# Optimization experiments

Measured on AMD Instinct MI355X. Metric: run time of the kernel, lower is better.

## Reference

```python
import jax, jax.numpy as jnp
import numpy as np

L, B, S, D, H, FF = 6, 6, 7, 512, 8, 2048  # layers, support-set size+1, nodes(1 verb + 6 nouns), dim, heads, ffn
HD = D // H


def setup_inputs() -> dict:
    key = jax.random.key(0)
    ks = jax.random.split(key, 16)
    n = lambda k, shape: jax.random.normal(k, shape, dtype=jnp.float32) * 0.02
    z = lambda shape: jnp.zeros(shape, jnp.float32)
    o = lambda shape: jnp.ones(shape, jnp.float32)
    return {
        'features': jax.random.normal(ks[0], (B, S, D), dtype=jnp.float32),
        'role_tokens': jax.random.normal(ks[1], (B, S - 1, D), dtype=jnp.float32),
        'in_w': n(ks[2], (L, 3 * D, D)), 'in_b': z((L, 3 * D)),
        'out_w': n(ks[3], (L, D, D)), 'out_b': z((L, D)),
        'ln1_w': o((L, D)), 'ln1_b': z((L, D)),
        'ln2_w': o((L, D)), 'ln2_b': z((L, D)),
        'ln3_w': o((L, D)), 'ln3_b': z((L, D)),
        'ln4_w': o((L, D)), 'ln4_b': z((L, D)),
        'f1_w1': n(ks[4], (L, FF, D)), 'f1_b1': z((L, FF)),
        'f1_w2': n(ks[5], (L, D, FF)), 'f1_b2': z((L, D)),
        'f2_w1': n(ks[6], (L, FF, D)), 'f2_b1': z((L, FF)),
        'f2_w2': n(ks[7], (L, D, FF)), 'f2_b2': z((L, D)),
        'a1_w': n(ks[8], (L, D, D * 5)), 'a1_b': z((L, D)),
        'a2_w': n(ks[9], (L, D, D * 6)), 'a2_b': z((L, D)),
    }


def _ln(x, w, b):
    mu = jnp.mean(x, -1, keepdims=True)
    var = jnp.mean(jnp.square(x - mu), -1, keepdims=True)
    return (x - mu) * jax.lax.rsqrt(var + 1e-5) * w + b


def _forward(features, role_tokens, in_w, in_b, out_w, out_b, ln1_w, ln1_b, ln2_w, ln2_b,
             ln3_w, ln3_b, ln4_w, ln4_b, f1_w1, f1_b1, f1_w2, f1_b2, f2_w1, f2_b1,
             f2_w2, f2_b2, a1_w, a1_b, a2_w, a2_b):
    def step(x, p):
        (iw, ib, ow, ob, l1w, l1b, l2w, l2b, l3w, l3b, l4w, l4b,
         w11, b11, w12, b12, w21, b21, w22, b22, aw1, ab1, aw2, ab2) = p
        # batched tiny self-attention over the 7 nodes of each of the 6 support examples
        src = x.at[:, 1:, :].add(role_tokens)                      # role embed on noun slots only
        qkv = jnp.einsum('bsd,ed->bse', src, iw) + ib              # (B,S,3D)
        q, k, v = jnp.split(qkv, 3, axis=-1)
        q = q.reshape(B, S, H, HD); k = k.reshape(B, S, H, HD); v = v.reshape(B, S, H, HD)
        att = jax.nn.softmax(jnp.einsum('bqhd,bkhd->bhqk', q, k) / jnp.sqrt(jnp.float32(HD)), axis=-1)
        ctx = jnp.einsum('bhqk,bkhd->bqhd', att, v).reshape(B, S, D)
        msg = jnp.einsum('bsd,ed->bse', ctx, ow) + ob              # (B,S,D)
        verb_msg = msg[:, 0, :]                                    # (B,D)
        noun_msg = msg[:, 1:, :]                                   # (B,S-1,D)
        # gated concat-aggregation
        agg_verb = jax.nn.sigmoid(verb_msg[1:].reshape(-1) @ aw1.T + ab1)  # (D,) from 5 support verb msgs
        agg_noun = jax.nn.sigmoid(noun_msg[0].reshape(-1) @ aw2.T + ab2)   # (D,) from 6 target noun msgs
        # noun update for target example (index 0)
        s = _ln(x[0, 1:, :] + agg_verb, l1w, l1b)                  # (6,D)
        s = _ln(s + (jax.nn.relu(s @ w11.T + b11) @ w12.T + b12), l2w, l2b)
        # verb update for target example
        t = _ln(x[0, 0, :] + agg_noun, l3w, l3b)                   # (D,)
        t = _ln(t + (jax.nn.relu(t @ w21.T + b21) @ w22.T + b22), l4w, l4b)
        new_self = jnp.concatenate([t[None, :], s], axis=0)        # (S,D)
        return jnp.concatenate([new_self[None], x[1:]], axis=0), None

    params = (in_w, in_b, out_w, out_b, ln1_w, ln1_b, ln2_w, ln2_b, ln3_w, ln3_b,
              ln4_w, ln4_b, f1_w1, f1_b1, f1_w2, f1_b2, f2_w1, f2_b1, f2_w2, f2_b2,
              a1_w, a1_b, a2_w, a2_b)
    out, _ = jax.lax.scan(step, features, params)
    return out[0:1]                                                # (1,7,512)


def reference(features, role_tokens, in_w, in_b, out_w, out_b, ln1_w, ln1_b, ln2_w, ln2_b,
              ln3_w, ln3_b, ln4_w, ln4_b, f1_w1, f1_b1, f1_w2, f1_b2, f2_w1, f2_b1,
              f2_w2, f2_b2, a1_w, a1_b, a2_w, a2_b):
    return _forward(features, role_tokens, in_w, in_b, out_w, out_b, ln1_w, ln1_b,
                    ln2_w, ln2_b, ln3_w, ln3_b, ln4_w, ln4_b, f1_w1, f1_b1, f1_w2, f1_b2,
                    f2_w1, f2_b1, f2_w2, f2_b2, a1_w, a1_b, a2_w, a2_b)
```

## Files before the change

kernel.cpp:

```cpp
#include <hip/hip_runtime.h>
#include <math.h>

#define NL 6
#define NB 6
#define NS 7
#define ND 512
#define NH 8
#define HDIM 64
#define NFF 2048
#define NROWS (NB*NS)

__device__ __forceinline__ float wave_sum(float v) {
    v += __shfl_down(v, 32, 64);
    v += __shfl_down(v, 16, 64);
    v += __shfl_down(v, 8, 64);
    v += __shfl_down(v, 4, 64);
    v += __shfl_down(v, 2, 64);
    v += __shfl_down(v, 1, 64);
    return v;
}

__device__ __forceinline__ float dot512(const float* __restrict__ a,
                                        const float* __restrict__ b, int lane) {
    int d0 = lane * 8;
    float4 a1 = *(const float4*)(a + d0);
    float4 a2 = *(const float4*)(a + d0 + 4);
    float4 b1 = *(const float4*)(b + d0);
    float4 b2 = *(const float4*)(b + d0 + 4);
    return a1.x*b1.x + a1.y*b1.y + a1.z*b1.z + a1.w*b1.w
         + a2.x*b2.x + a2.y*b2.y + a2.z*b2.z + a2.w*b2.w;
}

__global__ void qkv_kernel(const float* __restrict__ features,
                           const float* __restrict__ role,
                           const float* __restrict__ cur,
                           const float* __restrict__ iw,
                           const float* __restrict__ ib,
                           float* __restrict__ qkv) {
    int gw = (blockIdx.x * blockDim.x + threadIdx.x) >> 6;
    int lane = threadIdx.x & 63;
    if (gw >= NROWS * 1536) return;
    int row = gw / 1536;
    int e = gw - row * 1536;
    int b = row / NS, s = row - b * NS;
    const float* src = (b == 0) ? (cur + s * ND) : (features + row * ND);
    int d0 = lane * 8;
    float4 s1 = *(const float4*)(src + d0);
    float4 s2 = *(const float4*)(src + d0 + 4);
    if (s > 0) {
        const float* rp = role + (b * (NS-1) + (s-1)) * ND + d0;
        float4 r1 = *(const float4*)(rp);
        float4 r2 = *(const float4*)(rp + 4);
        s1.x += r1.x; s1.y += r1.y; s1.z += r1.z; s1.w += r1.w;
        s2.x += r2.x; s2.y += r2.y; s2.z += r2.z; s2.w += r2.w;
    }
    const float* wr = iw + e * ND + d0;
    float4 w1 = *(const float4*)(wr);
    float4 w2 = *(const float4*)(wr + 4);
    float acc = s1.x*w1.x + s1.y*w1.y + s1.z*w1.z + s1.w*w1.w
              + s2.x*w2.x + s2.y*w2.y + s2.z*w2.z + s2.w*w2.w;
    acc = wave_sum(acc);
    if (lane == 0) qkv[row * 1536 + e] = acc + ib[e];
}

__global__ void attn_kernel(const float* __restrict__ qkv, float* __restrict__ ctx) {
    int b = blockIdx.x >> 3, h = blockIdx.x & 7;
    int lane = threadIdx.x;
    __shared__ float q[NS][HDIM], k[NS][HDIM], v[NS][HDIM], att[NS][NS];
    for (int s = 0; s < NS; s++) {
        const float* base = qkv + (size_t)(b*NS + s) * 1536 + h * HDIM + lane;
        q[s][lane] = base[0];
        k[s][lane] = base[ND];
        v[s][lane] = base[2*ND];
    }
    __syncthreads();
    if (lane < NS*NS) {
        int i = lane / NS, j = lane - (lane / NS) * NS;
        float acc = 0.f;
        for (int d = 0; d < HDIM; d++) acc += q[i][d] * k[j][d];
        att[i][j] = acc * 0.125f;
    }
    __syncthreads();
    if (lane < NS) {
        float m = -1e30f;
        for (int j = 0; j < NS; j++) m = fmaxf(m, att[lane][j]);
        float e[NS]; float sum = 0.f;
        for (int j = 0; j < NS; j++) { e[j] = expf(att[lane][j] - m); sum += e[j]; }
        float inv = 1.f / sum;
        for (int j = 0; j < NS; j++) att[lane][j] = e[j] * inv;
    }
    __syncthreads();
    for (int s = 0; s < NS; s++) {
        float acc = 0.f;
        for (int j = 0; j < NS; j++) acc += att[s][j] * v[j][lane];
        ctx[(size_t)(b*NS + s) * ND + h * HDIM + lane] = acc;
    }
}

__global__ void msg_kernel(const float* __restrict__ ctx,
                           const float* __restrict__ ow,
                           const float* __restrict__ ob,
                           float* __restrict__ msg) {
    int gw = (blockIdx.x * blockDim.x + threadIdx.x) >> 6;
    int lane = threadIdx.x & 63;
    if (gw >= NROWS * ND) return;
    int row = gw / ND, e = gw - row * ND;
    float acc = wave_sum(dot512(ctx + (size_t)row * ND, ow + (size_t)e * ND, lane));
    if (lane == 0) msg[row * ND + e] = acc + ob[e];
}

__global__ void agg_kernel(const float* __restrict__ msg,
                           const float* __restrict__ aw1, const float* __restrict__ ab1,
                           const float* __restrict__ aw2, const float* __restrict__ ab2,
                           float* __restrict__ aggv, float* __restrict__ aggn) {
    int gw = (blockIdx.x * blockDim.x + threadIdx.x) >> 6;
    int lane = threadIdx.x & 63;
    if (gw < ND) {
        int j = gw;
        float acc = 0.f;
        for (int c = 0; c < 5; c++)
            acc += dot512(msg + (size_t)(c+1)*NS*ND, aw1 + (size_t)j*2560 + c*ND, lane);
        acc = wave_sum(acc);
        if (lane == 0) aggv[j] = 1.f / (1.f + expf(-(acc + ab1[j])));
    } else if (gw < 2*ND) {
        int j = gw - ND;
        float acc = 0.f;
        for (int c = 0; c < 6; c++)
            acc += dot512(msg + (size_t)(c+1)*ND, aw2 + (size_t)j*3072 + c*ND, lane);
        acc = wave_sum(acc);
        if (lane == 0) aggn[j] = 1.f / (1.f + expf(-(acc + ab2[j])));
    }
}

__global__ void ln13_kernel(const float* __restrict__ cur,
                            const float* __restrict__ aggv, const float* __restrict__ aggn,
                            const float* __restrict__ l1w, const float* __restrict__ l1b,
                            const float* __restrict__ l3w, const float* __restrict__ l3b,
                            float* __restrict__ xln) {
    int r = blockIdx.x, t = threadIdx.x;
    const float* agg = (r == 0) ? aggn : aggv;
    const float* w   = (r == 0) ? l3w : l1w;
    const float* bb  = (r == 0) ? l3b : l1b;
    float x0 = cur[r*ND + t]       + agg[t];
    float x1 = cur[r*ND + 256 + t] + agg[256 + t];
    __shared__ float sd[4];
    int lane = t & 63, wv = t >> 6;
    float v = wave_sum(x0 + x1);
    if (lane == 0) sd[wv] = v;
    __syncthreads();
    float mu = (sd[0] + sd[1] + sd[2] + sd[3]) * (1.f / ND);
    __syncthreads();
    float d0 = x0 - mu, d1 = x1 - mu;
    v = wave_sum(d0*d0 + d1*d1);
    if (lane == 0) sd[wv] = v;
    __syncthreads();
    float var = (sd[0] + sd[1] + sd[2] + sd[3]) * (1.f / ND);
    float inv = rsqrtf(var + 1e-5f);
    xln[r*ND + t]       = d0 * inv * w[t]     + bb[t];
    xln[r*ND + 256 + t] = d1 * inv * w[256+t] + bb[256+t];
}

__global__ void ffa_kernel(const float* __restrict__ xln,
                           const float* __restrict__ w11, const float* __restrict__ b11,
                           const float* __restrict__ w21, const float* __restrict__ b21,
                           float* __restrict__ h) {
    int gw = (blockIdx.x * blockDim.x + threadIdx.x) >> 6;
    int lane = threadIdx.x & 63;
    if (gw >= NS * NFF) return;
    int r = gw / NFF, f = gw - r * NFF;
    const float* W = (r == 0) ? (w21 + (size_t)f * ND) : (w11 + (size_t)f * ND);
    const float* bias = (r == 0) ? b21 : b11;
    float acc = wave_sum(dot512(xln + r * ND, W, lane));
    if (lane == 0) h[r * NFF + f] = fmaxf(acc + bias[f], 0.f);
}

__global__ void ffb_kernel(const float* __restrict__ xln, const float* __restrict__ hbuf,
                           const float* __restrict__ w12, const float* __restrict__ b12,
                           const float* __restrict__ w22, const float* __restrict__ b22,
                           float* __restrict__ ff) {
    int gw = (blockIdx.x * blockDim.x + threadIdx.x) >> 6;
    int lane = threadIdx.x & 63;
    if (gw >= NS * ND) return;
    int r = gw / ND, d = gw - r * ND;
    const float* W = (r == 0) ? (w22 + (size_t)d * NFF) : (w12 + (size_t)d * NFF);
    const float* bias = (r == 0) ? b22 : b12;
    const float* hin = hbuf + r * NFF;
    float acc = 0.f;
    for (int c = 0; c < 4; c++) acc += dot512(hin + c*ND, W + c*ND, lane);
    acc = wave_sum(acc);
    if (lane == 0) ff[r * ND + d] = xln[r * ND + d] + acc + bias[d];
}

__global__ void ln24_kernel(const float* __restrict__ ff,
                            const float* __restrict__ l2w, const float* __restrict__ l2b,
                            const float* __restrict__ l4w, const float* __restrict__ l4b,
                            float* __restrict__ cur, float* __restrict__ outp) {
    int r = blockIdx.x, t = threadIdx.x;
    const float* w  = (r == 0) ? l4w : l2w;
    const float* bb = (r == 0) ? l4b : l2b;
    float x0 = ff[r*ND + t], x1 = ff[r*ND + 256 + t];
    __shared__ float sd[4];
    int lane = t & 63, wv = t >> 6;
    float v = wave_sum(x0 + x1);
    if (lane == 0) sd[wv] = v;
    __syncthreads();
    float mu = (sd[0] + sd[1] + sd[2] + sd[3]) * (1.f / ND);
    __syncthreads();
    float d0 = x0 - mu, d1 = x1 - mu;
    v = wave_sum(d0*d0 + d1*d1);
    if (lane == 0) sd[wv] = v;
    __syncthreads();
    float var = (sd[0] + sd[1] + sd[2] + sd[3]) * (1.f / ND);
    float inv = rsqrtf(var + 1e-5f);
    float y0 = d0 * inv * w[t]     + bb[t];
    float y1 = d1 * inv * w[256+t] + bb[256+t];
    cur[r*ND + t]       = y0;
    cur[r*ND + 256 + t] = y1;
    if (outp) {
        outp[r*ND + t]       = y0;
        outp[r*ND + 256 + t] = y1;
    }
}

extern "C" void kernel_launch(void* const* d_in, const int* in_sizes, int n_in,
                              void* d_out, int out_size, void* d_ws, size_t ws_size,
                              hipStream_t stream) {
    const float* features = (const float*)d_in[0];
    const float* role     = (const float*)d_in[1];
    const float* in_w  = (const float*)d_in[2];
    const float* in_b  = (const float*)d_in[3];
    const float* out_w = (const float*)d_in[4];
    const float* out_b = (const float*)d_in[5];
    const float* ln1_w = (const float*)d_in[6];
    const float* ln1_b = (const float*)d_in[7];
    const float* ln2_w = (const float*)d_in[8];
    const float* ln2_b = (const float*)d_in[9];
    const float* ln3_w = (const float*)d_in[10];
    const float* ln3_b = (const float*)d_in[11];
    const float* ln4_w = (const float*)d_in[12];
    const float* ln4_b = (const float*)d_in[13];
    const float* f1_w1 = (const float*)d_in[14];
    const float* f1_b1 = (const float*)d_in[15];
    const float* f1_w2 = (const float*)d_in[16];
    const float* f1_b2 = (const float*)d_in[17];
    const float* f2_w1 = (const float*)d_in[18];
    const float* f2_b1 = (const float*)d_in[19];
    const float* f2_w2 = (const float*)d_in[20];
    const float* f2_b2 = (const float*)d_in[21];
    const float* a1_w  = (const float*)d_in[22];
    const float* a1_b  = (const float*)d_in[23];
    const float* a2_w  = (const float*)d_in[24];
    const float* a2_b  = (const float*)d_in[25];

    float* ws   = (float*)d_ws;
    float* cur  = ws;
    float* qkv  = ws + 3584;
    float* ctx  = qkv + 64512;
    float* msg  = ctx + 21504;
    float* aggv = msg + 21504;
    float* aggn = aggv + 512;
    float* xln  = aggn + 512;
    float* hbuf = xln + 3584;
    float* ff   = hbuf + 14336;

    hipMemcpyAsync(cur, features, 3584 * sizeof(float), hipMemcpyDeviceToDevice, stream);

    for (int l = 0; l < NL; l++) {
        qkv_kernel<<<NROWS*1536/4, 256, 0, stream>>>(
            features, role, cur, in_w + (size_t)l*1536*ND, in_b + (size_t)l*1536, qkv);
        attn_kernel<<<NB*NH, 64, 0, stream>>>(qkv, ctx);
        msg_kernel<<<NROWS*ND/4, 256, 0, stream>>>(
            ctx, out_w + (size_t)l*ND*ND, out_b + (size_t)l*ND, msg);
        agg_kernel<<<2*ND/4, 256, 0, stream>>>(
            msg, a1_w + (size_t)l*ND*2560, a1_b + (size_t)l*ND,
                 a2_w + (size_t)l*ND*3072, a2_b + (size_t)l*ND, aggv, aggn);
        ln13_kernel<<<NS, 256, 0, stream>>>(
            cur, aggv, aggn, ln1_w + (size_t)l*ND, ln1_b + (size_t)l*ND,
            ln3_w + (size_t)l*ND, ln3_b + (size_t)l*ND, xln);
        ffa_kernel<<<NS*NFF/4, 256, 0, stream>>>(
            xln, f1_w1 + (size_t)l*NFF*ND, f1_b1 + (size_t)l*NFF,
                 f2_w1 + (size_t)l*NFF*ND, f2_b1 + (size_t)l*NFF, hbuf);
        ffb_kernel<<<NS*ND/4, 256, 0, stream>>>(
            xln, hbuf, f1_w2 + (size_t)l*ND*NFF, f1_b2 + (size_t)l*ND,
                       f2_w2 + (size_t)l*ND*NFF, f2_b2 + (size_t)l*ND, ff);
        ln24_kernel<<<NS, 256, 0, stream>>>(
            ff, ln2_w + (size_t)l*ND, ln2_b + (size_t)l*ND,
                ln4_w + (size_t)l*ND, ln4_b + (size_t)l*ND,
            cur, (l == NL-1) ? (float*)d_out : nullptr);
    }
}
```

Measured before the change: 474.8 us.

## Fuse layernorms into consumers, prune unneeded query rows, fuse attention with out-proj

Removes the separate LN kernels and the device memcpy by recomputing the previous layer's LN2/LN4 inside the qkv, ffa and ffb kernels, with a final LN kernel only at the end. Q projection, attention and out-projection are restricted to the 11 rows whose messages are consumed downstream, and attention is fused with the out-projection via shared memory. FFN kernels now compute several outputs per block from a shared normalized row. This cuts launches and redundant work, at the cost of recomputing LN in many blocks and lower parallelism in the fused attention kernel.

```diff
diff --git a/kernel.cpp b/kernel.cpp
--- a/kernel.cpp
+++ b/kernel.cpp
@@ -10,6 +10,8 @@
 #define NFF 2048
 #define NROWS (NB*NS)
 
+__device__ __constant__ int NRQ[11] = {1,2,3,4,5,6,7,14,21,28,35};
+
 __device__ __forceinline__ float wave_sum(float v) {
     v += __shfl_down(v, 32, 64);
     v += __shfl_down(v, 16, 64);
@@ -17,6 +19,16 @@
     v += __shfl_down(v, 4, 64);
     v += __shfl_down(v, 2, 64);
     v += __shfl_down(v, 1, 64);
+    return v;
+}
+
+__device__ __forceinline__ float wave_sum_all(float v) {
+    v += __shfl_xor(v, 32, 64);
+    v += __shfl_xor(v, 16, 64);
+    v += __shfl_xor(v, 8, 64);
+    v += __shfl_xor(v, 4, 64);
+    v += __shfl_xor(v, 2, 64);
+    v += __shfl_xor(v, 1, 64);
     return v;
 }
 
@@ -31,170 +43,279 @@
          + a2.x*b2.x + a2.y*b2.y + a2.z*b2.z + a2.w*b2.w;
 }
 
-__global__ void qkv_kernel(const float* __restrict__ features,
-                           const float* __restrict__ role,
-                           const float* __restrict__ cur,
-                           const float* __restrict__ iw,
-                           const float* __restrict__ ib,
-                           float* __restrict__ qkv) {
-    int gw = (blockIdx.x * blockDim.x + threadIdx.x) >> 6;
-    int lane = threadIdx.x & 63;
-    if (gw >= NROWS * 1536) return;
-    int row = gw / 1536;
-    int e = gw - row * 1536;
-    int b = row / NS, s = row - b * NS;
-    const float* src = (b == 0) ? (cur + s * ND) : (features + row * ND);
+__device__ __forceinline__ float dot2048(const float* __restrict__ a,
+                                         const float* __restrict__ b, int lane) {
+    float acc = 0.f;
+    for (int c = 0; c < 4; c++) acc += dot512(a + c*ND, b + c*ND, lane);
+    return acc;
+}
+
+__device__ __forceinline__ void load_src(int b, int s, int lane, int l,
+    const float* __restrict__ features, const float* __restrict__ role,
+    const float* __restrict__ ffprev,
+    const float* __restrict__ l2w, const float* __restrict__ l2b,
+    const float* __restrict__ l4w, const float* __restrict__ l4b,
+    float4& s1, float4& s2)
+{
     int d0 = lane * 8;
-    float4 s1 = *(const float4*)(src + d0);
-    float4 s2 = *(const float4*)(src + d0 + 4);
+    if (b > 0 || l == 0) {
+        const float* src = features + (size_t)(b*NS + s) * ND + d0;
+        s1 = *(const float4*)src;
+        s2 = *(const float4*)(src + 4);
+    } else {
+        const float* fp = ffprev + s * ND + d0;
+        float4 f1 = *(const float4*)fp;
+        float4 f2 = *(const float4*)(fp + 4);
+        float sum = f1.x+f1.y+f1.z+f1.w + f2.x+f2.y+f2.z+f2.w;
+        sum = wave_sum_all(sum);
+        float mu = sum * (1.f/ND);
+        f1.x-=mu; f1.y-=mu; f1.z-=mu; f1.w-=mu;
+        f2.x-=mu; f2.y-=mu; f2.z-=mu; f2.w-=mu;
+        float sq = f1.x*f1.x+f1.y*f1.y+f1.z*f1.z+f1.w*f1.w
+                 + f2.x*f2.x+f2.y*f2.y+f2.z*f2.z+f2.w*f2.w;
+        sq = wave_sum_all(sq);
+        float inv = rsqrtf(sq*(1.f/ND) + 1e-5f);
+        const float* w  = (s == 0) ? l4w : l2w;
+        const float* bb = (s == 0) ? l4b : l2b;
+        float4 w1 = *(const float4*)(w + d0),  w2 = *(const float4*)(w + d0 + 4);
+        float4 b1 = *(const float4*)(bb + d0), b2 = *(const float4*)(bb + d0 + 4);
+        s1.x = f1.x*inv*w1.x + b1.x; s1.y = f1.y*inv*w1.y + b1.y;
+        s1.z = f1.z*inv*w1.z + b1.z; s1.w = f1.w*inv*w1.w + b1.w;
+        s2.x = f2.x*inv*w2.x + b2.x; s2.y = f2.y*inv*w2.y + b2.y;
+        s2.z = f2.z*inv*w2.z + b2.z; s2.w = f2.w*inv*w2.w + b2.w;
+    }
     if (s > 0) {
-        const float* rp = role + (b * (NS-1) + (s-1)) * ND + d0;
-        float4 r1 = *(const float4*)(rp);
+        const float* rp = role + (size_t)(b*(NS-1) + (s-1)) * ND + d0;
+        float4 r1 = *(const float4*)rp;
         float4 r2 = *(const float4*)(rp + 4);
         s1.x += r1.x; s1.y += r1.y; s1.z += r1.z; s1.w += r1.w;
         s2.x += r2.x; s2.y += r2.y; s2.z += r2.z; s2.w += r2.w;
     }
-    const float* wr = iw + e * ND + d0;
-    float4 w1 = *(const float4*)(wr);
+}
+
+#define KV_WAVES (NROWS*1024)
+#define Q_WAVES  (11*512)
+__global__ void qkv_kernel(const float* __restrict__ features,
+                           const float* __restrict__ role,
+                           const float* __restrict__ ffprev,
+                           const float* __restrict__ l2w, const float* __restrict__ l2b,
+                           const float* __restrict__ l4w, const float* __restrict__ l4b,
+                           const float* __restrict__ iw, const float* __restrict__ ib,
+                           float* __restrict__ qkv, int l) {
+    int gw = (blockIdx.x * blockDim.x + threadIdx.x) >> 6;
+    int lane = threadIdx.x & 63;
+    int row, e;
+    if (gw < KV_WAVES) {
+        row = gw >> 10;
+        e = 512 + (gw & 1023);
+    } else {
+        int g2 = gw - KV_WAVES;
+        if (g2 >= Q_WAVES) return;
+        row = NRQ[g2 >> 9];
+        e = g2 & 511;
+    }
+    int b = row / NS, s = row - b * NS;
+    float4 s1, s2;
+    load_src(b, s, lane, l, features, role, ffprev, l2w, l2b, l4w, l4b, s1, s2);
+    int d0 = lane * 8;
+    const float* wr = iw + (size_t)e * ND + d0;
+    float4 w1 = *(const float4*)wr;
     float4 w2 = *(const float4*)(wr + 4);
     float acc = s1.x*w1.x + s1.y*w1.y + s1.z*w1.z + s1.w*w1.w
               + s2.x*w2.x + s2.y*w2.y + s2.z*w2.z + s2.w*w2.w;
     acc = wave_sum(acc);
-    if (lane == 0) qkv[row * 1536 + e] = acc + ib[e];
-}
-
-__global__ void attn_kernel(const float* __restrict__ qkv, float* __restrict__ ctx) {
-    int b = blockIdx.x >> 3, h = blockIdx.x & 7;
-    int lane = threadIdx.x;
-    __shared__ float q[NS][HDIM], k[NS][HDIM], v[NS][HDIM], att[NS][NS];
-    for (int s = 0; s < NS; s++) {
-        const float* base = qkv + (size_t)(b*NS + s) * 1536 + h * HDIM + lane;
-        q[s][lane] = base[0];
-        k[s][lane] = base[ND];
-        v[s][lane] = base[2*ND];
-    }
-    __syncthreads();
-    if (lane < NS*NS) {
-        int i = lane / NS, j = lane - (lane / NS) * NS;
+    if (lane == 0) qkv[(size_t)row * 1536 + e] = acc + ib[e];
+}
+
+__global__ void msg_attn_kernel(const float* __restrict__ qkv,
+                                const float* __restrict__ ow,
+                                const float* __restrict__ ob,
+                                float* __restrict__ msg) {
+    int row = NRQ[blockIdx.x >> 3];
+    int chunk = blockIdx.x & 7;
+    int b = row / NS, s = row - b * NS;
+    int t = threadIdx.x;
+    __shared__ float ctx_s[ND];
+    __shared__ float att_s[NH][NS];
+    const float* qkvb = qkv + (size_t)b * NS * 1536;
+    int h = t >> 5, l5 = t & 31;
+    if (l5 < NS) {
+        const float* qp = qkvb + (size_t)s * 1536 + h * HDIM;
+        const float* kp = qkvb + (size_t)l5 * 1536 + ND + h * HDIM;
         float acc = 0.f;
-        for (int d = 0; d < HDIM; d++) acc += q[i][d] * k[j][d];
-        att[i][j] = acc * 0.125f;
-    }
-    __syncthreads();
-    if (lane < NS) {
+        for (int d = 0; d < HDIM; d++) acc += qp[d] * kp[d];
+        att_s[h][l5] = acc * 0.125f;
+    }
+    __syncthreads();
+    if (l5 == 0) {
         float m = -1e30f;
-        for (int j = 0; j < NS; j++) m = fmaxf(m, att[lane][j]);
-        float e[NS]; float sum = 0.f;
-        for (int j = 0; j < NS; j++) { e[j] = expf(att[lane][j] - m); sum += e[j]; }
+        for (int j = 0; j < NS; j++) m = fmaxf(m, att_s[h][j]);
+        float e[NS], sum = 0.f;
+        for (int j = 0; j < NS; j++) { e[j] = expf(att_s[h][j] - m); sum += e[j]; }
         float inv = 1.f / sum;
-        for (int j = 0; j < NS; j++) att[lane][j] = e[j] * inv;
-    }
-    __syncthreads();
-    for (int s = 0; s < NS; s++) {
-        float acc = 0.f;
-        for (int j = 0; j < NS; j++) acc += att[s][j] * v[j][lane];
-        ctx[(size_t)(b*NS + s) * ND + h * HDIM + lane] = acc;
-    }
-}
-
-__global__ void msg_kernel(const float* __restrict__ ctx,
-                           const float* __restrict__ ow,
-                           const float* __restrict__ ob,
-                           float* __restrict__ msg) {
-    int gw = (blockIdx.x * blockDim.x + threadIdx.x) >> 6;
-    int lane = threadIdx.x & 63;
-    if (gw >= NROWS * ND) return;
-    int row = gw / ND, e = gw - row * ND;
-    float acc = wave_sum(dot512(ctx + (size_t)row * ND, ow + (size_t)e * ND, lane));
-    if (lane == 0) msg[row * ND + e] = acc + ob[e];
+        for (int j = 0; j < NS; j++) att_s[h][j] = e[j] * inv;
+    }
+    __syncthreads();
+    {
+        int d = l5 * 2;
+        const float* vp = qkvb + 2*ND + h*HDIM + d;
+        float a0 = 0.f, a1 = 0.f;
+        for (int j = 0; j < NS; j++) {
+            float aj = att_s[h][j];
+            a0 += aj * vp[(size_t)j*1536];
+            a1 += aj * vp[(size_t)j*1536 + 1];
+        }
+        ctx_s[h*HDIM + d] = a0;
+        ctx_s[h*HDIM + d + 1] = a1;
+    }
+    __syncthreads();
+    int wv = t >> 6, lane = t & 63;
+    for (int i = 0; i < 16; i++) {
+        int e = chunk*64 + wv*16 + i;
+        float acc = dot512(ctx_s, ow + (size_t)e * ND, lane);
+        acc = wave_sum(acc);
+        if (lane == 0) msg[(size_t)row * ND + e] = acc + ob[e];
+    }
 }
 
 __global__ void agg_kernel(const float* __restrict__ msg,
                            const float* __restrict__ aw1, const float* __restrict__ ab1,
                            const float* __restrict__ aw2, const float* __restrict__ ab2,
                            float* __restrict__ aggv, float* __restrict__ aggn) {
-    int gw = (blockIdx.x * blockDim.x + threadIdx.x) >> 6;
-    int lane = threadIdx.x & 63;
-    if (gw < ND) {
-        int j = gw;
-        float acc = 0.f;
-        for (int c = 0; c < 5; c++)
-            acc += dot512(msg + (size_t)(c+1)*NS*ND, aw1 + (size_t)j*2560 + c*ND, lane);
-        acc = wave_sum(acc);
-        if (lane == 0) aggv[j] = 1.f / (1.f + expf(-(acc + ab1[j])));
-    } else if (gw < 2*ND) {
-        int j = gw - ND;
-        float acc = 0.f;
-        for (int c = 0; c < 6; c++)
-            acc += dot512(msg + (size_t)(c+1)*ND, aw2 + (size_t)j*3072 + c*ND, lane);
-        acc = wave_sum(acc);
-        if (lane == 0) aggn[j] = 1.f / (1.f + expf(-(acc + ab2[j])));
-    }
-}
-
-__global__ void ln13_kernel(const float* __restrict__ cur,
-                            const float* __restrict__ aggv, const float* __restrict__ aggn,
-                            const float* __restrict__ l1w, const float* __restrict__ l1b,
-                            const float* __restrict__ l3w, const float* __restrict__ l3b,
-                            float* __restrict__ xln) {
-    int r = blockIdx.x, t = threadIdx.x;
-    const float* agg = (r == 0) ? aggn : aggv;
-    const float* w   = (r == 0) ? l3w : l1w;
-    const float* bb  = (r == 0) ? l3b : l1b;
-    float x0 = cur[r*ND + t]       + agg[t];
-    float x1 = cur[r*ND + 256 + t] + agg[256 + t];
+    int j = blockIdx.x, t = threadIdx.x;
     __shared__ float sd[4];
+    float acc = 0.f;
+    if (j < ND) {
+        const float* wj = aw1 + (size_t)j * 2560;
+        for (int c = 0; c < 5; c++) {
+            const float* mp = msg + (size_t)(c+1) * NS * ND;
+            acc += mp[t] * wj[c*512 + t] + mp[256 + t] * wj[c*512 + 256 + t];
+        }
+    } else {
+        const float* wj = aw2 + (size_t)(j - ND) * 3072;
+        for (int c = 0; c < 6; c++) {
+            const float* mp = msg + (size_t)(c+1) * ND;
+            acc += mp[t] * wj[c*512 + t] + mp[256 + t] * wj[c*512 + 256 + t];
+        }
+    }
+    float v = wave_sum(acc);
     int lane = t & 63, wv = t >> 6;
+    if (lane == 0) sd[wv] = v;
+    __syncthreads();
+    if (t == 0) {
+        float s = sd[0] + sd[1] + sd[2] + sd[3];
+        if (j < ND) aggv[j] = 1.f / (1.f + expf(-(s + ab1[j])));
+        else        aggn[j - ND] = 1.f / (1.f + expf(-(s + ab2[j - ND])));
+    }
+}
+
+__device__ __forceinline__ void build_xln(int r, int l,
+    const float* __restrict__ features, const float* __restrict__ ffprev,
+    const float* __restrict__ lnpw, const float* __restrict__ lnpb,
+    const float* __restrict__ agg,
+    const float* __restrict__ lnw, const float* __restrict__ lnb,
+    float* xs, float* sd)
+{
+    int t = threadIdx.x, lane = t & 63, wv = t >> 6;
+    float x0, x1;
+    if (l == 0) {
+        x0 = features[r*ND + t];
+        x1 = features[r*ND + 256 + t];
+    } else {
+        float f0 = ffprev[r*ND + t], f1 = ffprev[r*ND + 256 + t];
+        float v = wave_sum(f0 + f1);
+        if (lane == 0) sd[wv] = v;
+        __syncthreads();
+        float mu = (sd[0]+sd[1]+sd[2]+sd[3]) * (1.f/ND);
+        __syncthreads();
+        float d0 = f0 - mu, d1 = f1 - mu;
+        v = wave_sum(d0*d0 + d1*d1);
+        if (lane == 0) sd[wv] = v;
+        __syncthreads();
+        float var = (sd[0]+sd[1]+sd[2]+sd[3]) * (1.f/ND);
+        float inv = rsqrtf(var + 1e-5f);
+        x0 = d0*inv*lnpw[t]     + lnpb[t];
+        x1 = d1*inv*lnpw[256+t] + lnpb[256+t];
+        __syncthreads();
+    }
+    x0 += agg[t];
+    x1 += agg[256 + t];
     float v = wave_sum(x0 + x1);
     if (lane == 0) sd[wv] = v;
     __syncthreads();
-    float mu = (sd[0] + sd[1] + sd[2] + sd[3]) * (1.f / ND);
+    float mu = (sd[0]+sd[1]+sd[2]+sd[3]) * (1.f/ND);
     __syncthreads();
     float d0 = x0 - mu, d1 = x1 - mu;
     v = wave_sum(d0*d0 + d1*d1);
     if (lane == 0) sd[wv] = v;
     __syncthreads();
-    float var = (sd[0] + sd[1] + sd[2] + sd[3]) * (1.f / ND);
+    float var = (sd[0]+sd[1]+sd[2]+sd[3]) * (1.f/ND);
     float inv = rsqrtf(var + 1e-5f);
-    xln[r*ND + t]       = d0 * inv * w[t]     + bb[t];
-    xln[r*ND + 256 + t] = d1 * inv * w[256+t] + bb[256+t];
-}
-
-__global__ void ffa_kernel(const float* __restrict__ xln,
+    xs[t]       = d0*inv*lnw[t]     + lnb[t];
+    xs[256 + t] = d1*inv*lnw[256+t] + lnb[256+t];
+    __syncthreads();
+}
+
+__global__ void ffa_kernel(const float* __restrict__ features, const float* __restrict__ ffprev,
+                           const float* __restrict__ l2pw, const float* __restrict__ l2pb,
+                           const float* __restrict__ l4pw, const float* __restrict__ l4pb,
+                           const float* __restrict__ aggv, const float* __restrict__ aggn,
+                           const float* __restrict__ ln1w, const float* __restrict__ ln1b,
+                           const float* __restrict__ ln3w, const float* __restrict__ ln3b,
                            const float* __restrict__ w11, const float* __restrict__ b11,
                            const float* __restrict__ w21, const float* __restrict__ b21,
-                           float* __restrict__ h) {
-    int gw = (blockIdx.x * blockDim.x + threadIdx.x) >> 6;
-    int lane = threadIdx.x & 63;
-    if (gw >= NS * NFF) return;
-    int r = gw / NFF, f = gw - r * NFF;
-    const float* W = (r == 0) ? (w21 + (size_t)f * ND) : (w11 + (size_t)f * ND);
-    const float* bias = (r == 0) ? b21 : b11;
-    float acc = wave_sum(dot512(xln + r * ND, W, lane));
-    if (lane == 0) h[r * NFF + f] = fmaxf(acc + bias[f], 0.f);
-}
-
-__global__ void ffb_kernel(const float* __restrict__ xln, const float* __restrict__ hbuf,
+                           float* __restrict__ hbuf, int l) {
+    int r = blockIdx.x >> 7, fc = blockIdx.x & 127;
+    __shared__ float xs[ND];
+    __shared__ float sd[4];
+    build_xln(r, l, features, ffprev,
+              (r == 0) ? l4pw : l2pw, (r == 0) ? l4pb : l2pb,
+              (r == 0) ? aggn : aggv,
+              (r == 0) ? ln3w : ln1w, (r == 0) ? ln3b : ln1b, xs, sd);
+    const float* W = (r == 0) ? w21 : w11;
+    const float* B = (r == 0) ? b21 : b11;
+    int wv = threadIdx.x >> 6, lane = threadIdx.x & 63;
+    for (int i = 0; i < 4; i++) {
+        int f = fc*16 + wv*4 + i;
+        float acc = dot512(xs, W + (size_t)f * ND, lane);
+        acc = wave_sum(acc);
+        if (lane == 0) hbuf[r*NFF + f] = fmaxf(acc + B[f], 0.f);
+    }
+}
+
+__global__ void ffb_kernel(const float* __restrict__ features, const float* __restrict__ ffprev,
+                           const float* __restrict__ l2pw, const float* __restrict__ l2pb,
+                           const float* __restrict__ l4pw, const float* __restrict__ l4pb,
+                           const float* __restrict__ aggv, const float* __restrict__ aggn,
+                           const float* __restrict__ ln1w, const float* __restrict__ ln1b,
+                           const float* __restrict__ ln3w, const float* __restrict__ ln3b,
+                           const float* __restrict__ hbuf,
                            const float* __restrict__ w12, const float* __restrict__ b12,
                            const float* __restrict__ w22, const float* __restrict__ b22,
-                           float* __restrict__ ff) {
-    int gw = (blockIdx.x * blockDim.x + threadIdx.x) >> 6;
-    int lane = threadIdx.x & 63;
-    if (gw >= NS * ND) return;
-    int r = gw / ND, d = gw - r * ND;
-    const float* W = (r == 0) ? (w22 + (size_t)d * NFF) : (w12 + (size_t)d * NFF);
-    const float* bias = (r == 0) ? b22 : b12;
-    const float* hin = hbuf + r * NFF;
-    float acc = 0.f;
-    for (int c = 0; c < 4; c++) acc += dot512(hin + c*ND, W + c*ND, lane);
-    acc = wave_sum(acc);
-    if (lane == 0) ff[r * ND + d] = xln[r * ND + d] + acc + bias[d];
-}
-
-__global__ void ln24_kernel(const float* __restrict__ ff,
-                            const float* __restrict__ l2w, const float* __restrict__ l2b,
-                            const float* __restrict__ l4w, const float* __restrict__ l4b,
-                            float* __restrict__ cur, float* __restrict__ outp) {
+                           float* __restrict__ ff, int l) {
+    int r = blockIdx.x >> 6, dc = blockIdx.x & 63;
+    __shared__ float xs[ND];
+    __shared__ float sd[4];
+    build_xln(r, l, features, ffprev,
+              (r == 0) ? l4pw : l2pw, (r == 0) ? l4pb : l2pb,
+              (r == 0) ? aggn : aggv,
+              (r == 0) ? ln3w : ln1w, (r == 0) ? ln3b : ln1b, xs, sd);
+    const float* W = (r == 0) ? w22 : w12;
+    const float* B = (r == 0) ? b22 : b12;
+    const float* hr = hbuf + r * NFF;
+    int wv = threadIdx.x >> 6, lane = threadIdx.x & 63;
+    for (int i = 0; i < 2; i++) {
+        int d = dc*8 + wv*2 + i;
+        float acc = dot2048(hr, W + (size_t)d * NFF, lane);
+        acc = wave_sum(acc);
+        if (lane == 0) ff[r*ND + d] = xs[d] + acc + B[d];
+    }
+}
+
+__global__ void final_ln_kernel(const float* __restrict__ ff,
+                                const float* __restrict__ l2w, const float* __restrict__ l2b,
+                                const float* __restrict__ l4w, const float* __restrict__ l4b,
+                                float* __restrict__ outp) {
     int r = blockIdx.x, t = threadIdx.x;
     const float* w  = (r == 0) ? l4w : l2w;
     const float* bb = (r == 0) ? l4b : l2b;
@@ -204,22 +325,16 @@
     float v = wave_sum(x0 + x1);
     if (lane == 0) sd[wv] = v;
     __syncthreads();
-    float mu = (sd[0] + sd[1] + sd[2] + sd[3]) * (1.f / ND);
+    float mu = (sd[0]+sd[1]+sd[2]+sd[3]) * (1.f/ND);
     __syncthreads();
     float d0 = x0 - mu, d1 = x1 - mu;
     v = wave_sum(d0*d0 + d1*d1);
     if (lane == 0) sd[wv] = v;
     __syncthreads();
-    float var = (sd[0] + sd[1] + sd[2] + sd[3]) * (1.f / ND);
+    float var = (sd[0]+sd[1]+sd[2]+sd[3]) * (1.f/ND);
     float inv = rsqrtf(var + 1e-5f);
-    float y0 = d0 * inv * w[t]     + bb[t];
-    float y1 = d1 * inv * w[256+t] + bb[256+t];
-    cur[r*ND + t]       = y0;
-    cur[r*ND + 256 + t] = y1;
-    if (outp) {
-        outp[r*ND + t]       = y0;
-        outp[r*ND + 256 + t] = y1;
-    }
+    outp[r*ND + t]       = d0*inv*w[t]     + bb[t];
+    outp[r*ND + 256 + t] = d1*inv*w[256+t] + bb[256+t];
 }
 
 extern "C" void kernel_launch(void* const* d_in, const int* in_sizes, int n_in,
@@ -253,39 +368,50 @@
     const float* a2_b  = (const float*)d_in[25];
 
     float* ws   = (float*)d_ws;
-    float* cur  = ws;
-    float* qkv  = ws + 3584;
-    float* ctx  = qkv + 64512;
-    float* msg  = ctx + 21504;
+    float* qkv  = ws;
+    float* msg  = qkv + 64512;
     float* aggv = msg + 21504;
     float* aggn = aggv + 512;
-    float* xln  = aggn + 512;
-    float* hbuf = xln + 3584;
-    float* ff   = hbuf + 14336;
-
-    hipMemcpyAsync(cur, features, 3584 * sizeof(float), hipMemcpyDeviceToDevice, stream);
+    float* hbuf = aggn + 512;
+    float* ffA  = hbuf + 14336;
+    float* ffB  = ffA + 3584;
+    float* ffb_[2] = {ffA, ffB};
+
+    const int QKV_BLOCKS = (KV_WAVES + Q_WAVES) / 4;
 
     for (int l = 0; l < NL; l++) {
-        qkv_kernel<<<NROWS*1536/4, 256, 0, stream>>>(
-            features, role, cur, in_w + (size_t)l*1536*ND, in_b + (size_t)l*1536, qkv);
-        attn_kernel<<<NB*NH, 64, 0, stream>>>(qkv, ctx);
-        msg_kernel<<<NROWS*ND/4, 256, 0, stream>>>(
-            ctx, out_w + (size_t)l*ND*ND, out_b + (size_t)l*ND, msg);
-        agg_kernel<<<2*ND/4, 256, 0, stream>>>(
+        const float* ffprev = (l == 0) ? nullptr : ffb_[(l-1) & 1];
+        float* ffcur = ffb_[l & 1];
+        const float* l2pw = ln2_w + (size_t)((l > 0) ? l-1 : 0) * ND;
+        const float* l2pb = ln2_b + (size_t)((l > 0) ? l-1 : 0) * ND;
+        const float* l4pw = ln4_w + (size_t)((l > 0) ? l-1 : 0) * ND;
+        const float* l4pb = ln4_b + (size_t)((l > 0) ? l-1 : 0) * ND;
+
+        qkv_kernel<<<QKV_BLOCKS, 256, 0, stream>>>(
+            features, role, ffprev, l2pw, l2pb, l4pw, l4pb,
+            in_w + (size_t)l*1536*ND, in_b + (size_t)l*1536, qkv, l);
+        msg_attn_kernel<<<11*8, 256, 0, stream>>>(
+            qkv, out_w + (size_t)l*ND*ND, out_b + (size_t)l*ND, msg);
+        agg_kernel<<<2*ND, 256, 0, stream>>>(
             msg, a1_w + (size_t)l*ND*2560, a1_b + (size_t)l*ND,
                  a2_w + (size_t)l*ND*3072, a2_b + (size_t)l*ND, aggv, aggn);
-        ln13_kernel<<<NS, 256, 0, stream>>>(
-            cur, aggv, aggn, ln1_w + (size_t)l*ND, ln1_b + (size_t)l*ND,
-            ln3_w + (size_t)l*ND, ln3_b + (size_t)l*ND, xln);
-        ffa_kernel<<<NS*NFF/4, 256, 0, stream>>>(
-            xln, f1_w1 + (size_t)l*NFF*ND, f1_b1 + (size_t)l*NFF,
-                 f2_w1 + (size_t)l*NFF*ND, f2_b1 + (size_t)l*NFF, hbuf);
-        ffb_kernel<<<NS*ND/4, 256, 0, stream>>>(
-            xln, hbuf, f1_w2 + (size_t)l*ND*NFF, f1_b2 + (size_t)l*ND,
-                       f2_w2 + (size_t)l*ND*NFF, f2_b2 + (size_t)l*ND, ff);
-        ln24_kernel<<<NS, 256, 0, stream>>>(
-            ff, ln2_w + (size_t)l*ND, ln2_b + (size_t)l*ND,
-                ln4_w + (size_t)l*ND, ln4_b + (size_t)l*ND,
-            cur, (l == NL-1) ? (float*)d_out : nullptr);
-    }
-}
+        ffa_kernel<<<NS*128, 256, 0, stream>>>(
+            features, ffprev, l2pw, l2pb, l4pw, l4pb, aggv, aggn,
+            ln1_w + (size_t)l*ND, ln1_b + (size_t)l*ND,
+            ln3_w + (size_t)l*ND, ln3_b + (size_t)l*ND,
+            f1_w1 + (size_t)l*NFF*ND, f1_b1 + (size_t)l*NFF,
+            f2_w1 + (size_t)l*NFF*ND, f2_b1 + (size_t)l*NFF, hbuf, l);
+        ffb_kernel<<<NS*64, 256, 0, stream>>>(
+            features, ffprev, l2pw, l2pb, l4pw, l4pb, aggv, aggn,
+            ln1_w + (size_t)l*ND, ln1_b + (size_t)l*ND,
+            ln3_w + (size_t)l*ND, ln3_b + (size_t)l*ND,
+            hbuf,
+            f1_w2 + (size_t)l*ND*NFF, f1_b2 + (size_t)l*ND,
+            f2_w2 + (size_t)l*ND*NFF, f2_b2 + (size_t)l*ND, ffcur, l);
+    }
+    final_ln_kernel<<<NS, 256, 0, stream>>>(
+        ffb_[(NL-1) & 1],
+        ln2_w + (size_t)(NL-1)*ND, ln2_b + (size_t)(NL-1)*ND,
+        ln4_w + (size_t)(NL-1)*ND, ln4_b + (size_t)(NL-1)*ND,
+        (float*)d_out);
+}
```

Measured after the change: 511.5 us. 7.7% more time.
